# Performance work log

Hardware: AMD Instinct MI355X
Metric: run time of the kernel (lower is better)

Reference implementation:

```python
import jax, jax.numpy as jnp
import numpy as np

BN_EPS = 1e-5
LEAKY_SLOPE = 0.01

def setup_inputs() -> dict:
    key = jax.random.key(0)
    ks = jax.random.split(key, 8)
    B, N, C, D = 8, 2048, 128, 32  # batch, points, inchannels, outchannels
    s = 0.05
    return {
        "x": jax.random.normal(ks[0], (B, N, C), dtype=jnp.float32),
        "Wq": jax.random.normal(ks[1], (D, C), dtype=jnp.float32) * s,
        "Wk": jax.random.normal(ks[2], (D, C), dtype=jnp.float32) * s,
        "Wv": jax.random.normal(ks[3], (C, C), dtype=jnp.float32) * s,
        "Wp": jax.random.normal(ks[4], (C, C), dtype=jnp.float32) * s,
        "bn_gamma": jnp.ones((C,), dtype=jnp.float32),
        "bn_beta": jnp.zeros((C,), dtype=jnp.float32),
        "bn_mean": jax.random.normal(ks[5], (C,), dtype=jnp.float32) * 0.01,
        "bn_var": jnp.abs(jax.random.normal(ks[6], (C,), dtype=jnp.float32)) * 0.1 + 0.9,
    }

def reference(x, Wq, Wk, Wv, Wp, bn_gamma, bn_beta, bn_mean, bn_var):
    # x: [B, N, C]; 1x1 Conv1d == per-point linear map
    q = jnp.einsum('bnc,dc->bnd', x, Wq)          # [B, N, D]
    k = jnp.einsum('bnc,dc->bnd', x, Wk)          # [B, N, D]
    v = jnp.einsum('bnc,oc->bno', x, Wv)          # [B, N, C]
    energy = jnp.einsum('bnd,bmd->bnm', q, k)     # [B, Nq, Nk]
    # offset-attention: softmax over the QUERY axis (dim=1), then L1-renorm over keys
    attn = jax.nn.softmax(energy, axis=1)
    attn = attn / (1e-9 + attn.sum(axis=-1, keepdims=True))
    x_r = jnp.einsum('bnm,bmc->bnc', attn, v)     # [B, N, C]
    # project(x - x_r): 1x1 conv + BatchNorm (eval, running stats) + LeakyReLU; dropout p=0
    d = x - x_r
    y = jnp.einsum('bnc,oc->bno', d, Wp)
    y = (y - bn_mean) * (bn_gamma / jnp.sqrt(bn_var + BN_EPS)) + bn_beta
    y = jnp.where(y >= 0, y, LEAKY_SLOPE * y)
    return y + x
```

## Files before the change

kernel.cpp:

```cpp
#include <hip/hip_runtime.h>
#include <stdint.h>

#define BB 8
#define NN 2048
#define CC 128
#define DD 32
#define LOG2E 1.44269504088896340736f

typedef __attribute__((ext_vector_type(8))) short short8;
typedef __attribute__((ext_vector_type(4))) short short4v;
typedef __attribute__((ext_vector_type(4))) float f32x4;

#define MFMA(a,b,c) __builtin_amdgcn_mfma_f32_16x16x32_bf16(a,b,c,0,0,0)

__device__ __forceinline__ f32x4 MFMA16(short4v a, short4v b, f32x4 c){
#if __has_builtin(__builtin_amdgcn_mfma_f32_16x16x16bf16_1k)
  return __builtin_amdgcn_mfma_f32_16x16x16bf16_1k(a, b, c, 0, 0, 0);
#else
  f32x4 d;
  asm volatile("s_nop 1\n\tv_mfma_f32_16x16x16_bf16 %0, %1, %2, %3\n\ts_nop 4"
               : "=&v"(d) : "v"(a), "v"(b), "v"(c));
  return d;
#endif
}

__device__ __forceinline__ short f2b(float f){
  uint32_t u = __float_as_uint(f);
  uint32_t r = (u + 0x7fffu + ((u >> 16) & 1u)) >> 16;
  return (short)r;
}
__device__ __forceinline__ float b2f(short s){
  uint32_t u = ((uint32_t)(uint16_t)s) << 16;
  return __uint_as_float(u);
}

__global__ __launch_bounds__(256,4) void k_qkv(const float* __restrict__ x,
    const float* __restrict__ Wq, const float* __restrict__ Wk, const float* __restrict__ Wv,
    short* __restrict__ qb, short* __restrict__ kb, short* __restrict__ vt){
  const int tid = threadIdx.x;
  const int wv = tid >> 6, l = tid & 63, lrow = l & 15, lg = l >> 4;
  const int r0 = blockIdx.x*16;
  const int base = wv*3;
  const float* xr = x + (long)(r0 + lrow)*CC;
  short8 a[4];
  #pragma unroll
  for (int ks=0; ks<4; ks++){
    f32x4 u0 = *(const f32x4*)(xr + ks*32 + lg*8);
    f32x4 u1 = *(const f32x4*)(xr + ks*32 + lg*8 + 4);
    short8 t;
    #pragma unroll
    for (int j=0;j<4;j++){ t[j] = f2b(u0[j]); t[4+j] = f2b(u1[j]); }
    a[ks] = t;
  }
  f32x4 acc[3];
  #pragma unroll
  for (int i=0;i<3;i++) acc[i] = f32x4{0.f,0.f,0.f,0.f};
  #pragma unroll
  for (int of=0; of<3; of++){
    const int oo = base + of;
    const int row = oo*16 + lrow;
    const float* Wr = (oo < 2) ? (Wq + row*CC) : (oo < 4) ? (Wk + (row-32)*CC) : (Wv + (row-64)*CC);
    #pragma unroll
    for (int ks=0; ks<4; ks++){
      f32x4 w0 = *(const f32x4*)(Wr + ks*32 + lg*8);
      f32x4 w1 = *(const f32x4*)(Wr + ks*32 + lg*8 + 4);
      short8 bfr;
      #pragma unroll
      for (int j=0;j<4;j++){ bfr[j] = f2b(w0[j]); bfr[4+j] = f2b(w1[j]); }
      acc[of] = MFMA(a[ks], bfr, acc[of]);
    }
  }
  const int b = r0 / NN, nin = r0 % NN;
  #pragma unroll
  for (int of=0; of<3; of++){
    const int oo = base + of;
    const int o = oo*16 + lrow;
    if (oo < 2){
      #pragma unroll
      for (int rr=0; rr<4; rr++) qb[(long)(r0 + lg*4 + rr)*DD + o] = f2b(acc[of][rr]*LOG2E);
    } else if (oo < 4){
      #pragma unroll
      for (int rr=0; rr<4; rr++) kb[(long)(r0 + lg*4 + rr)*DD + (o-32)] = f2b(acc[of][rr]);
    } else {
      short4v s;
      #pragma unroll
      for (int rr=0; rr<4; rr++) s[rr] = f2b(acc[of][rr]);
      *(short4v*)(vt + (long)(b*CC + (o-64))*NN + nin + lg*4) = s;
    }
  }
}

__global__ __launch_bounds__(256,4) void k_colsum(const short* __restrict__ qb, const short* __restrict__ kb,
                                                  float* __restrict__ csum){
  const int tid = threadIdx.x;
  const int wv = tid >> 6, l = tid & 63, lrow = l & 15, lg = l >> 4;
  const int bq = blockIdx.x & 31;
  const int b = bq >> 2, q = bq & 3;
  const int m0 = (blockIdx.x >> 5)*64 + wv*16;
  short8 afr = *(const short8*)(kb + (long)(b*NN + m0 + lrow)*DD + lg*8);
  const short* qbase = qb + (long)b*NN*DD;
  float sum[4] = {0.f,0.f,0.f,0.f};
  f32x4 z = {0.f,0.f,0.f,0.f};
  const int nbeg = q*512, nend = nbeg + 512;
  #pragma unroll 4
  for (int n0=nbeg; n0<nend; n0+=16){
    short8 bfr = *(const short8*)(qbase + (long)(n0 + lrow)*DD + lg*8);
    f32x4 e = MFMA(afr, bfr, z);
    #pragma unroll
    for (int r=0;r<4;r++) sum[r] += exp2f(e[r]);
  }
  #pragma unroll
  for (int mask=1; mask<16; mask<<=1){
    #pragma unroll
    for (int r=0;r<4;r++) sum[r] += __shfl_xor(sum[r], mask);
  }
  if (lrow == 0){
    #pragma unroll
    for (int r=0;r<4;r++) csum[q*(BB*NN) + b*NN + m0 + lg*4 + r] = sum[r];
  }
}

__global__ __launch_bounds__(256,2) void k_attn(const short* __restrict__ qb,
    const short* __restrict__ kb, const short* __restrict__ vt, const float* __restrict__ csum,
    short* __restrict__ accPb, float* __restrict__ Lp){
  __shared__ __align__(16) short lds[16896];
  const int tid = threadIdx.x;
  const int kw = tid >> 6, l = tid & 63, lrow = l & 15, lg = l >> 4;
  const int bq = blockIdx.x & 31;
  const int b = bq >> 2;
  const int quarter = bq & 3;
  const int rt = blockIdx.x >> 5;
  const int n0 = rt*64;
  const short* kbb = kb + (long)b*NN*DD;
  const short* vtb = vt + (long)b*CC*NN;
  float* sinvl = (float*)(lds + 11776);

  short8 qfr[4];
  #pragma unroll
  for (int rg=0; rg<4; rg++)
    qfr[rg] = *(const short8*)(qb + (long)(b*NN + n0 + rg*16 + lrow)*DD + lg*8);

  const int mbase = quarter*512;
  {
    const float* c0p = csum + b*NN + mbase;
    #pragma unroll
    for (int i=tid; i<512; i+=256){
      float s = c0p[i] + c0p[i + BB*NN] + c0p[i + 2*BB*NN] + c0p[i + 3*BB*NN];
      sinvl[i] = __builtin_amdgcn_rcpf(s);
    }
  }

  f32x4 acc[4][8];
  #pragma unroll
  for (int rg=0; rg<4; rg++)
    #pragma unroll
    for (int i=0;i<8;i++) acc[rg][i] = f32x4{0.f,0.f,0.f,0.f};
  float Lacc[4] = {0.f,0.f,0.f,0.f};

  short8 sv[4]; short8 sk[2];
  const int cr = tid >> 1, hf = tid & 1;
  auto loadT = [&](int m0){
    const short* s = vtb + (long)cr*NN + m0 + hf*32;
    sv[0] = *(const short8*)(s);
    sv[1] = *(const short8*)(s+8);
    sv[2] = *(const short8*)(s+16);
    sv[3] = *(const short8*)(s+24);
    if (tid < 128){
      const short* s2 = kbb + (long)(m0 + cr)*DD + hf*16;
      sk[0] = *(const short8*)(s2);
      sk[1] = *(const short8*)(s2+8);
    }
  };
  auto storeT = [&](){
    *(short8*)(lds + cr*72 + hf*32 + 0)  = sv[0];
    *(short8*)(lds + cr*72 + hf*32 + 8)  = sv[1];
    *(short8*)(lds + cr*72 + hf*32 + 16) = sv[2];
    *(short8*)(lds + cr*72 + hf*32 + 24) = sv[3];
    if (tid < 128){
      short* kb_t = lds + 9216;
      *(short8*)(kb_t + cr*40 + hf*16 + 0) = sk[0];
      *(short8*)(kb_t + cr*40 + hf*16 + 8) = sk[1];
    }
  };

  loadT(mbase);
  storeT();
  __syncthreads();

  f32x4 z = {0.f,0.f,0.f,0.f};
  for (int it=0; it<8; it++){
    if (it < 7) loadT(mbase + it*64 + 64);
    short8 kfr = *(short8*)(lds + 9216 + (kw*16 + lrow)*40 + lg*8);
    float si[4];
    #pragma unroll
    for (int r=0;r<4;r++) si[r] = sinvl[it*64 + kw*16 + lg*4 + r];
    short4v vbf[8];
    #pragma unroll
    for (int cf=0; cf<8; cf++)
      vbf[cf] = *(short4v*)(lds + (cf*16 + lrow)*72 + kw*16 + lg*4);
    __builtin_amdgcn_s_setprio(1);
    #pragma unroll
    for (int rg=0; rg<4; rg++){
      f32x4 e = MFMA(kfr, qfr[rg], z);
      float p0 = exp2f(e[0])*si[0], p1 = exp2f(e[1])*si[1];
      float p2 = exp2f(e[2])*si[2], p3 = exp2f(e[3])*si[3];
      Lacc[rg] += (p0+p1) + (p2+p3);
      short4v pa; pa[0]=f2b(p0); pa[1]=f2b(p1); pa[2]=f2b(p2); pa[3]=f2b(p3);
      #pragma unroll
      for (int cf=0; cf<8; cf++)
        acc[rg][cf] = MFMA16(pa, vbf[cf], acc[rg][cf]);
    }
    __builtin_amdgcn_s_setprio(0);
    __syncthreads();
    if (it < 7){
      storeT();
      __syncthreads();
    }
  }

  const long tile = (long)((b*32 + rt)*4 + quarter);

  float Lr[4];
  #pragma unroll
  for (int rg=0; rg<4; rg++){
    float v = Lacc[rg];
    v += __shfl_xor(v, 16);
    v += __shfl_xor(v, 32);
    Lr[rg] = v;
  }
  float* Lb = (float*)(lds + 16384);
  if (l < 16){
    #pragma unroll
    for (int rg=0; rg<4; rg++) Lb[kw*64 + rg*16 + l] = Lr[rg];
  }
  __syncthreads();
  if (l < 16){
    float s = Lb[kw*16 + l] + Lb[64 + kw*16 + l] + Lb[128 + kw*16 + l] + Lb[192 + kw*16 + l];
    Lp[tile*64 + kw*16 + l] = s;
  }

  for (int round=0; round<2; round++){
    const int c0 = round*2;
    #pragma unroll
    for (int cc=0; cc<2; cc++){
      short* dst = lds + (cc*4 + kw)*2048;
      const int c = c0 + cc;
      #pragma unroll
      for (int cf=0; cf<8; cf++)
        #pragma unroll
        for (int r=0;r<4;r++)
          dst[(lg*4+r)*128 + cf*16 + lrow] = f2b(acc[c][cf][r]);
    }
    __syncthreads();
    {
      const int cc = kw & 1;
      const int row = (kw>>1)*8 + (l>>3);
      const int cb = (l&7)*16;
      const short* src = lds + cc*8192 + row*128 + cb;
      float s[16];
      #pragma unroll
      for (int j=0;j<16;j++) s[j] = 0.f;
      #pragma unroll
      for (int slot=0; slot<4; slot++){
        short8 v0 = *(const short8*)(src + slot*2048);
        short8 v1 = *(const short8*)(src + slot*2048 + 8);
        #pragma unroll
        for (int j=0;j<8;j++){ s[j] += b2f(v0[j]); s[8+j] += b2f(v1[j]); }
      }
      short8 o0, o1;
      #pragma unroll
      for (int j=0;j<8;j++){ o0[j] = f2b(s[j]); o1[j] = f2b(s[8+j]); }
      short* aP = accPb + tile*64*128 + ((c0+cc)*16 + row)*128 + cb;
      *(short8*)aP = o0;
      *(short8*)(aP + 8) = o1;
    }
    __syncthreads();
  }
}

__global__ __launch_bounds__(256,4) void k_fin(const float* __restrict__ x, const short* __restrict__ accPb,
    const float* __restrict__ Lp, const float* __restrict__ Wp, const float* __restrict__ g,
    const float* __restrict__ bt, const float* __restrict__ mu, const float* __restrict__ vr,
    float* __restrict__ out){
  __shared__ __align__(16) short dl[16*136];
  __shared__ float linv_s[16];
  const int tid = threadIdx.x;
  const int wv = tid >> 6, l = tid & 63, lrow = l & 15, lg = l >> 4;
  const int b = blockIdx.x >> 7;
  const int rt = blockIdx.x & 127;
  const int nb = rt*16;
  const long tileIdx = (long)(b*32 + (rt>>2))*4;
  const int rowoff = (rt&3)*16;

  if (tid < 16){
    float Ls = Lp[(tileIdx+0)*64 + rowoff + tid] + Lp[(tileIdx+1)*64 + rowoff + tid]
             + Lp[(tileIdx+2)*64 + rowoff + tid] + Lp[(tileIdx+3)*64 + rowoff + tid];
    linv_s[tid] = __builtin_amdgcn_rcpf(1e-9f + Ls);
  }

  const int row_l = tid >> 4;
  const int c0 = (tid & 15)*8;
  float a[8];
  #pragma unroll
  for (int j=0;j<8;j++) a[j] = 0.f;
  #pragma unroll
  for (int p=0;p<4;p++){
    short8 v = *(const short8*)(accPb + (tileIdx+p)*64*128 + (rowoff+row_l)*128 + c0);
    #pragma unroll
    for (int j=0;j<8;j++) a[j] += b2f(v[j]);
  }
  const float* xr = x + ((long)(b*NN + nb + row_l))*CC + c0;
  f32x4 x0 = *(const f32x4*)(xr);
  f32x4 x1 = *(const f32x4*)(xr + 4);
  __syncthreads();
  {
    const float li = linv_s[row_l];
    short4v d0, d1;
    #pragma unroll
    for (int j=0;j<4;j++){
      d0[j] = f2b(x0[j] - a[j]*li);
      d1[j] = f2b(x1[j] - a[4+j]*li);
    }
    *(short4v*)(dl + row_l*136 + c0) = d0;
    *(short4v*)(dl + row_l*136 + c0 + 4) = d1;
  }
  __syncthreads();

  f32x4 yac[2];
  yac[0] = f32x4{0.f,0.f,0.f,0.f};
  yac[1] = f32x4{0.f,0.f,0.f,0.f};
  #pragma unroll
  for (int ks=0; ks<4; ks++){
    short8 da = *(short8*)(dl + lrow*136 + ks*32 + lg*8);
    #pragma unroll
    for (int of=0; of<2; of++){
      const float* wr = Wp + ((wv*2+of)*16 + lrow)*CC + ks*32 + lg*8;
      f32x4 w0 = *(const f32x4*)(wr);
      f32x4 w1 = *(const f32x4*)(wr + 4);
      short8 wfr;
      #pragma unroll
      for (int j=0;j<4;j++){ wfr[j] = f2b(w0[j]); wfr[4+j] = f2b(w1[j]); }
      yac[of] = MFMA(da, wfr, yac[of]);
    }
  }
  float* ob = out + ((long)(b*NN + nb))*CC;
  const float* xb = x + ((long)(b*NN + nb))*CC;
  #pragma unroll
  for (int of=0; of<2; of++){
    const int o = (wv*2+of)*16 + lrow;
    const float sc = g[o] * rsqrtf(vr[o] + 1e-5f);
    const float sh = bt[o] - mu[o]*sc;
    #pragma unroll
    for (int r=0;r<4;r++){
      float y = yac[of][r]*sc + sh;
      y = (y >= 0.f) ? y : 0.01f*y;
      ob[(lg*4+r)*CC + o] = y + xb[(lg*4+r)*CC + o];
    }
  }
}

extern "C" void kernel_launch(void* const* d_in, const int* in_sizes, int n_in,
                              void* d_out, int out_size, void* d_ws, size_t ws_size,
                              hipStream_t stream) {
  const float* x  = (const float*)d_in[0];
  const float* Wq = (const float*)d_in[1];
  const float* Wk = (const float*)d_in[2];
  const float* Wv = (const float*)d_in[3];
  const float* Wp = (const float*)d_in[4];
  const float* g  = (const float*)d_in[5];
  const float* bt = (const float*)d_in[6];
  const float* mu = (const float*)d_in[7];
  const float* vr = (const float*)d_in[8];
  float* out = (float*)d_out;

  char* ws = (char*)d_ws;
  short* qb    = (short*)(ws + 98304);
  short* kb    = (short*)(ws + 1146880);
  short* vt    = (short*)(ws + 2195456);
  float* csum  = (float*)(ws + 6389760);
  float* Lp    = (float*)(ws + 6651904);
  short* accPb = (short*)(ws + 6914048);

  k_qkv<<<1024, 256, 0, stream>>>(x, Wq, Wk, Wv, qb, kb, vt);
  k_colsum<<<1024, 256, 0, stream>>>(qb, kb, csum);
  k_attn<<<1024, 256, 0, stream>>>(qb, kb, vt, csum, accPb, Lp);
  k_fin<<<1024, 256, 0, stream>>>(x, accPb, Lp, Wp, g, bt, mu, vr, out);
}
```

Before: 145.4 us.

## Restructure attention kernel to per-wave query tiles and prepack bf16 weights

k_attn now gives each wave its own 32 query rows (128 per block, 512 blocks) instead of splitting keys across waves. Probabilities are staged through LDS so the P·V product can use the 16x16x32 MFMA, and the cross-wave LDS reduction of partial accumulators is gone. A new k_pack kernel converts the weights to bf16 once and precomputes the BatchNorm scale and shift, removing per-block conversion work in k_qkv and k_fin. The cost is an extra launch, more LDS (which may limit occupancy), and scattered 2-byte LDS writes of P.

```diff
diff --git a/kernel.cpp b/kernel.cpp
--- a/kernel.cpp
+++ b/kernel.cpp
@@ -13,17 +13,6 @@
 
 #define MFMA(a,b,c) __builtin_amdgcn_mfma_f32_16x16x32_bf16(a,b,c,0,0,0)
 
-__device__ __forceinline__ f32x4 MFMA16(short4v a, short4v b, f32x4 c){
-#if __has_builtin(__builtin_amdgcn_mfma_f32_16x16x16bf16_1k)
-  return __builtin_amdgcn_mfma_f32_16x16x16bf16_1k(a, b, c, 0, 0, 0);
-#else
-  f32x4 d;
-  asm volatile("s_nop 1\n\tv_mfma_f32_16x16x16_bf16 %0, %1, %2, %3\n\ts_nop 4"
-               : "=&v"(d) : "v"(a), "v"(b), "v"(c));
-  return d;
-#endif
-}
-
 __device__ __forceinline__ short f2b(float f){
   uint32_t u = __float_as_uint(f);
   uint32_t r = (u + 0x7fffu + ((u >> 16) & 1u)) >> 16;
@@ -34,8 +23,27 @@
   return __uint_as_float(u);
 }
 
-__global__ __launch_bounds__(256,4) void k_qkv(const float* __restrict__ x,
-    const float* __restrict__ Wq, const float* __restrict__ Wk, const float* __restrict__ Wv,
+__global__ void k_pack(const float* __restrict__ Wq, const float* __restrict__ Wk,
+                       const float* __restrict__ Wv, const float* __restrict__ Wp,
+                       const float* __restrict__ g, const float* __restrict__ bt,
+                       const float* __restrict__ mu, const float* __restrict__ vr,
+                       short* __restrict__ wqkv, short* __restrict__ wp,
+                       float* __restrict__ scale, float* __restrict__ shift){
+  int i = blockIdx.x*256 + threadIdx.x;
+  if (i < 192*128){
+    int r = i >> 7, c = i & 127;
+    float w = (r < 32) ? Wq[r*128+c] : (r < 64) ? Wk[(r-32)*128+c] : Wv[(r-64)*128+c];
+    wqkv[i] = f2b(w);
+  }
+  if (i < 128*128) wp[i] = f2b(Wp[i]);
+  if (i < 128){
+    float s = g[i] * rsqrtf(vr[i] + 1e-5f);
+    scale[i] = s;
+    shift[i] = bt[i] - mu[i]*s;
+  }
+}
+
+__global__ __launch_bounds__(256,4) void k_qkv(const float* __restrict__ x, const short* __restrict__ wqkv,
     short* __restrict__ qb, short* __restrict__ kb, short* __restrict__ vt){
   const int tid = threadIdx.x;
   const int wv = tid >> 6, l = tid & 63, lrow = l & 15, lg = l >> 4;
@@ -57,16 +65,9 @@
   for (int i=0;i<3;i++) acc[i] = f32x4{0.f,0.f,0.f,0.f};
   #pragma unroll
   for (int of=0; of<3; of++){
-    const int oo = base + of;
-    const int row = oo*16 + lrow;
-    const float* Wr = (oo < 2) ? (Wq + row*CC) : (oo < 4) ? (Wk + (row-32)*CC) : (Wv + (row-64)*CC);
     #pragma unroll
     for (int ks=0; ks<4; ks++){
-      f32x4 w0 = *(const f32x4*)(Wr + ks*32 + lg*8);
-      f32x4 w1 = *(const f32x4*)(Wr + ks*32 + lg*8 + 4);
-      short8 bfr;
-      #pragma unroll
-      for (int j=0;j<4;j++){ bfr[j] = f2b(w0[j]); bfr[4+j] = f2b(w1[j]); }
+      short8 bfr = *(const short8*)(wqkv + ((base+of)*16 + lrow)*CC + ks*32 + lg*8);
       acc[of] = MFMA(a[ks], bfr, acc[of]);
     }
   }
@@ -123,21 +124,21 @@
 __global__ __launch_bounds__(256,2) void k_attn(const short* __restrict__ qb,
     const short* __restrict__ kb, const short* __restrict__ vt, const float* __restrict__ csum,
     short* __restrict__ accPb, float* __restrict__ Lp){
-  __shared__ __align__(16) short lds[16896];
+  __shared__ __align__(16) short lds[22016];
   const int tid = threadIdx.x;
-  const int kw = tid >> 6, l = tid & 63, lrow = l & 15, lg = l >> 4;
+  const int wv = tid >> 6, l = tid & 63, lrow = l & 15, lg = l >> 4;
   const int bq = blockIdx.x & 31;
   const int b = bq >> 2;
   const int quarter = bq & 3;
   const int rt = blockIdx.x >> 5;
-  const int n0 = rt*64;
+  const int n0 = rt*128 + wv*32;
   const short* kbb = kb + (long)b*NN*DD;
   const short* vtb = vt + (long)b*CC*NN;
-  float* sinvl = (float*)(lds + 11776);
-
-  short8 qfr[4];
-  #pragma unroll
-  for (int rg=0; rg<4; rg++)
+  float* sinvl = (float*)(lds + 20992);
+
+  short8 qfr[2];
+  #pragma unroll
+  for (int rg=0; rg<2; rg++)
     qfr[rg] = *(const short8*)(qb + (long)(b*NN + n0 + rg*16 + lrow)*DD + lg*8);
 
   const int mbase = quarter*512;
@@ -150,12 +151,12 @@
     }
   }
 
-  f32x4 acc[4][8];
-  #pragma unroll
-  for (int rg=0; rg<4; rg++)
+  f32x4 acc[2][8];
+  #pragma unroll
+  for (int rg=0; rg<2; rg++)
     #pragma unroll
     for (int i=0;i<8;i++) acc[rg][i] = f32x4{0.f,0.f,0.f,0.f};
-  float Lacc[4] = {0.f,0.f,0.f,0.f};
+  float L[2][4] = {{0.f,0.f,0.f,0.f},{0.f,0.f,0.f,0.f}};
 
   short8 sv[4]; short8 sk[2];
   const int cr = tid >> 1, hf = tid & 1;
@@ -187,28 +188,41 @@
   storeT();
   __syncthreads();
 
+  short* pl = lds + 11776 + wv*2304;
   f32x4 z = {0.f,0.f,0.f,0.f};
   for (int it=0; it<8; it++){
     if (it < 7) loadT(mbase + it*64 + 64);
-    short8 kfr = *(short8*)(lds + 9216 + (kw*16 + lrow)*40 + lg*8);
-    float si[4];
-    #pragma unroll
-    for (int r=0;r<4;r++) si[r] = sinvl[it*64 + kw*16 + lg*4 + r];
-    short4v vbf[8];
-    #pragma unroll
-    for (int cf=0; cf<8; cf++)
-      vbf[cf] = *(short4v*)(lds + (cf*16 + lrow)*72 + kw*16 + lg*4);
+    short* kb_t = lds + 9216;
+    short8 kf[4];
+    #pragma unroll
+    for (int mt=0; mt<4; mt++)
+      kf[mt] = *(short8*)(kb_t + (mt*16 + lrow)*40 + lg*8);
+    #pragma unroll
+    for (int rg=0; rg<2; rg++){
+      #pragma unroll
+      for (int mt=0; mt<4; mt++){
+        f32x4 e = MFMA(qfr[rg], kf[mt], z);
+        float si = sinvl[it*64 + mt*16 + lrow];
+        float p0 = exp2f(e[0])*si, p1 = exp2f(e[1])*si;
+        float p2 = exp2f(e[2])*si, p3 = exp2f(e[3])*si;
+        L[rg][0] += p0; L[rg][1] += p1; L[rg][2] += p2; L[rg][3] += p3;
+        pl[(rg*16 + lg*4 + 0)*72 + mt*16 + lrow] = f2b(p0);
+        pl[(rg*16 + lg*4 + 1)*72 + mt*16 + lrow] = f2b(p1);
+        pl[(rg*16 + lg*4 + 2)*72 + mt*16 + lrow] = f2b(p2);
+        pl[(rg*16 + lg*4 + 3)*72 + mt*16 + lrow] = f2b(p3);
+      }
+    }
     __builtin_amdgcn_s_setprio(1);
     #pragma unroll
-    for (int rg=0; rg<4; rg++){
-      f32x4 e = MFMA(kfr, qfr[rg], z);
-      float p0 = exp2f(e[0])*si[0], p1 = exp2f(e[1])*si[1];
-      float p2 = exp2f(e[2])*si[2], p3 = exp2f(e[3])*si[3];
-      Lacc[rg] += (p0+p1) + (p2+p3);
-      short4v pa; pa[0]=f2b(p0); pa[1]=f2b(p1); pa[2]=f2b(p2); pa[3]=f2b(p3);
-      #pragma unroll
-      for (int cf=0; cf<8; cf++)
-        acc[rg][cf] = MFMA16(pa, vbf[cf], acc[rg][cf]);
+    for (int ks=0; ks<2; ks++){
+      short8 pa0 = *(short8*)(pl + (lrow)*72 + ks*32 + lg*8);
+      short8 pa1 = *(short8*)(pl + (16 + lrow)*72 + ks*32 + lg*8);
+      #pragma unroll
+      for (int cf=0; cf<8; cf++){
+        short8 vb_ = *(short8*)(lds + (cf*16 + lrow)*72 + ks*32 + lg*8);
+        acc[0][cf] = MFMA(pa0, vb_, acc[0][cf]);
+        acc[1][cf] = MFMA(pa1, vb_, acc[1][cf]);
+      }
     }
     __builtin_amdgcn_s_setprio(0);
     __syncthreads();
@@ -218,70 +232,35 @@
     }
   }
 
-  const long tile = (long)((b*32 + rt)*4 + quarter);
-
-  float Lr[4];
-  #pragma unroll
-  for (int rg=0; rg<4; rg++){
-    float v = Lacc[rg];
-    v += __shfl_xor(v, 16);
-    v += __shfl_xor(v, 32);
-    Lr[rg] = v;
-  }
-  float* Lb = (float*)(lds + 16384);
-  if (l < 16){
-    #pragma unroll
-    for (int rg=0; rg<4; rg++) Lb[kw*64 + rg*16 + l] = Lr[rg];
-  }
-  __syncthreads();
-  if (l < 16){
-    float s = Lb[kw*16 + l] + Lb[64 + kw*16 + l] + Lb[128 + kw*16 + l] + Lb[192 + kw*16 + l];
-    Lp[tile*64 + kw*16 + l] = s;
-  }
-
-  for (int round=0; round<2; round++){
-    const int c0 = round*2;
-    #pragma unroll
-    for (int cc=0; cc<2; cc++){
-      short* dst = lds + (cc*4 + kw)*2048;
-      const int c = c0 + cc;
-      #pragma unroll
-      for (int cf=0; cf<8; cf++)
-        #pragma unroll
-        for (int r=0;r<4;r++)
-          dst[(lg*4+r)*128 + cf*16 + lrow] = f2b(acc[c][cf][r]);
-    }
-    __syncthreads();
-    {
-      const int cc = kw & 1;
-      const int row = (kw>>1)*8 + (l>>3);
-      const int cb = (l&7)*16;
-      const short* src = lds + cc*8192 + row*128 + cb;
-      float s[16];
-      #pragma unroll
-      for (int j=0;j<16;j++) s[j] = 0.f;
-      #pragma unroll
-      for (int slot=0; slot<4; slot++){
-        short8 v0 = *(const short8*)(src + slot*2048);
-        short8 v1 = *(const short8*)(src + slot*2048 + 8);
-        #pragma unroll
-        for (int j=0;j<8;j++){ s[j] += b2f(v0[j]); s[8+j] += b2f(v1[j]); }
-      }
-      short8 o0, o1;
-      #pragma unroll
-      for (int j=0;j<8;j++){ o0[j] = f2b(s[j]); o1[j] = f2b(s[8+j]); }
-      short* aP = accPb + tile*64*128 + ((c0+cc)*16 + row)*128 + cb;
-      *(short8*)aP = o0;
-      *(short8*)(aP + 8) = o1;
-    }
-    __syncthreads();
-  }
+  #pragma unroll
+  for (int mask=1; mask<16; mask<<=1){
+    #pragma unroll
+    for (int rg=0; rg<2; rg++)
+      #pragma unroll
+      for (int r=0;r<4;r++) L[rg][r] += __shfl_xor(L[rg][r], mask);
+  }
+  const long tile = (long)((b*16 + rt)*4 + quarter);
+  if (lrow == 0){
+    #pragma unroll
+    for (int rg=0; rg<2; rg++)
+      #pragma unroll
+      for (int r=0;r<4;r++)
+        Lp[tile*128 + wv*32 + rg*16 + lg*4 + r] = L[rg][r];
+  }
+
+  short* aP = accPb + tile*128*128;
+  #pragma unroll
+  for (int rg=0; rg<2; rg++)
+    #pragma unroll
+    for (int cf=0; cf<8; cf++)
+      #pragma unroll
+      for (int r=0;r<4;r++)
+        aP[(wv*32 + rg*16 + lg*4 + r)*128 + cf*16 + lrow] = f2b(acc[rg][cf][r]);
 }
 
 __global__ __launch_bounds__(256,4) void k_fin(const float* __restrict__ x, const short* __restrict__ accPb,
-    const float* __restrict__ Lp, const float* __restrict__ Wp, const float* __restrict__ g,
-    const float* __restrict__ bt, const float* __restrict__ mu, const float* __restrict__ vr,
-    float* __restrict__ out){
+    const float* __restrict__ Lp, const short* __restrict__ wp, const float* __restrict__ scale,
+    const float* __restrict__ shift, float* __restrict__ out){
   __shared__ __align__(16) short dl[16*136];
   __shared__ float linv_s[16];
   const int tid = threadIdx.x;
@@ -289,12 +268,12 @@
   const int b = blockIdx.x >> 7;
   const int rt = blockIdx.x & 127;
   const int nb = rt*16;
-  const long tileIdx = (long)(b*32 + (rt>>2))*4;
-  const int rowoff = (rt&3)*16;
+  const long tileIdx = (long)(b*16 + (rt>>3))*4;
+  const int rowoff = (rt&7)*16;
 
   if (tid < 16){
-    float Ls = Lp[(tileIdx+0)*64 + rowoff + tid] + Lp[(tileIdx+1)*64 + rowoff + tid]
-             + Lp[(tileIdx+2)*64 + rowoff + tid] + Lp[(tileIdx+3)*64 + rowoff + tid];
+    float Ls = Lp[(tileIdx+0)*128 + rowoff + tid] + Lp[(tileIdx+1)*128 + rowoff + tid]
+             + Lp[(tileIdx+2)*128 + rowoff + tid] + Lp[(tileIdx+3)*128 + rowoff + tid];
     linv_s[tid] = __builtin_amdgcn_rcpf(1e-9f + Ls);
   }
 
@@ -305,7 +284,7 @@
   for (int j=0;j<8;j++) a[j] = 0.f;
   #pragma unroll
   for (int p=0;p<4;p++){
-    short8 v = *(const short8*)(accPb + (tileIdx+p)*64*128 + (rowoff+row_l)*128 + c0);
+    short8 v = *(const short8*)(accPb + (tileIdx+p)*128*128 + (rowoff+row_l)*128 + c0);
     #pragma unroll
     for (int j=0;j<8;j++) a[j] += b2f(v[j]);
   }
@@ -334,12 +313,7 @@
     short8 da = *(short8*)(dl + lrow*136 + ks*32 + lg*8);
     #pragma unroll
     for (int of=0; of<2; of++){
-      const float* wr = Wp + ((wv*2+of)*16 + lrow)*CC + ks*32 + lg*8;
-      f32x4 w0 = *(const f32x4*)(wr);
-      f32x4 w1 = *(const f32x4*)(wr + 4);
-      short8 wfr;
-      #pragma unroll
-      for (int j=0;j<4;j++){ wfr[j] = f2b(w0[j]); wfr[4+j] = f2b(w1[j]); }
+      short8 wfr = *(const short8*)(wp + ((wv*2+of)*16 + lrow)*CC + ks*32 + lg*8);
       yac[of] = MFMA(da, wfr, yac[of]);
     }
   }
@@ -348,8 +322,7 @@
   #pragma unroll
   for (int of=0; of<2; of++){
     const int o = (wv*2+of)*16 + lrow;
-    const float sc = g[o] * rsqrtf(vr[o] + 1e-5f);
-    const float sh = bt[o] - mu[o]*sc;
+    const float sc = scale[o], sh = shift[o];
     #pragma unroll
     for (int r=0;r<4;r++){
       float y = yac[of][r]*sc + sh;
@@ -374,6 +347,10 @@
   float* out = (float*)d_out;
 
   char* ws = (char*)d_ws;
+  short* wqkv  = (short*)(ws + 0);
+  short* wp    = (short*)(ws + 49152);
+  float* scale = (float*)(ws + 81920);
+  float* shift = (float*)(ws + 82432);
   short* qb    = (short*)(ws + 98304);
   short* kb    = (short*)(ws + 1146880);
   short* vt    = (short*)(ws + 2195456);
@@ -381,8 +358,9 @@
   float* Lp    = (float*)(ws + 6651904);
   short* accPb = (short*)(ws + 6914048);
 
-  k_qkv<<<1024, 256, 0, stream>>>(x, Wq, Wk, Wv, qb, kb, vt);
+  k_pack<<<96, 256, 0, stream>>>(Wq, Wk, Wv, Wp, g, bt, mu, vr, wqkv, wp, scale, shift);
+  k_qkv<<<1024, 256, 0, stream>>>(x, wqkv, qb, kb, vt);
   k_colsum<<<1024, 256, 0, stream>>>(qb, kb, csum);
-  k_attn<<<1024, 256, 0, stream>>>(qb, kb, vt, csum, accPb, Lp);
-  k_fin<<<1024, 256, 0, stream>>>(x, accPb, Lp, Wp, g, bt, mu, vr, out);
-}
+  k_attn<<<512, 256, 0, stream>>>(qb, kb, vt, csum, accPb, Lp);
+  k_fin<<<1024, 256, 0, stream>>>(x, accPb, Lp, wp, scale, shift, out);
+}
```

Result: faster. 131.9 us (-9.3%).
